# Kernel optimization log

Hardware: AMD Instinct MI355X
Metric: run time of the kernel (lower is better)

Reference implementation:

```python
import jax, jax.numpy as jnp
import numpy as np

N_SRC = 50000   # source nodes in the block
N_DST = 50000   # destination nodes
E = 800000      # edges (avg in-degree 16, every dst has >=1 edge)
D = 256         # hidden_dim
V = 50000       # vocab_size
C = 104         # n_classes (POJ-104)


def setup_inputs() -> dict:
    key = jax.random.key(0)
    k1, k2, k3, k4, k5, k6 = jax.random.split(key, 6)
    token_id = jax.random.randint(k1, (N_SRC,), 0, V, dtype=jnp.int32)
    src_idx = jax.random.randint(k2, (E,), 0, N_SRC, dtype=jnp.int32)
    # every dst node gets at least one in-edge (DGL raises on 0-in-degree),
    # remaining edges land on random dst nodes; sorted so edges are grouped by dst
    extra = jax.random.randint(k3, (E - N_DST,), 0, N_DST, dtype=jnp.int32)
    dst_idx = jnp.sort(jnp.concatenate([jnp.arange(N_DST, dtype=jnp.int32), extra]))
    emb = jax.random.normal(k4, (V, D), dtype=jnp.float32)  # nn.Embedding default N(0,1)
    W = jax.random.normal(k5, (D, D), dtype=jnp.float32) / jnp.sqrt(D)
    b = jnp.zeros((D,), dtype=jnp.float32)
    Wc = jax.random.normal(k6, (C, D), dtype=jnp.float32) / jnp.sqrt(D)
    bc = jnp.zeros((C,), dtype=jnp.float32)
    return {"emb": emb, "W": W, "b": b, "Wc": Wc, "bc": bc,
            "token_id": token_id, "src_idx": src_idx, "dst_idx": dst_idx}


def reference(emb, W, b, Wc, bc, token_id, src_idx, dst_idx):
    # embedding gather for source nodes (first_layer branch)
    feat_src = emb[token_id]                  # [N_SRC, D]
    # message: copy_u -> mailbox messages per edge
    msgs = feat_src[src_idx]                  # [E, D]
    # per-dst segment stats (dst_idx is sorted / grouped by dst)
    deg = jax.ops.segment_sum(jnp.ones((E,), dtype=jnp.int32), dst_idx,
                              num_segments=N_DST)            # [N_DST]
    sum_all = jax.ops.segment_sum(msgs, dst_idx, num_segments=N_DST)  # [N_DST, D]
    # DGL mailbox reducer: last message in the segment is the 'current input',
    # the rest are children summed through CodeRNNCell: x = cur + relu(W @ sum_children + b)
    last_idx = jnp.cumsum(deg) - 1            # index of last edge per dst segment
    last_msg = msgs[last_idx]                 # [N_DST, D]
    child_sum = sum_all - last_msg            # sum of msgs excluding the last one
    rnn_out = last_msg + jax.nn.relu(child_sum @ W.T + b)
    # length == 1 segments bypass the RNN cell entirely: ft = the single message
    ft = jnp.where((deg == 1)[:, None], last_msg, rnn_out)   # [N_DST, D]
    # final classifier
    return ft @ Wc.T + bc                     # [N_DST, C]
```

## Files before the change

kernel.cpp:

```cpp
#include <hip/hip_runtime.h>
#include <hip/hip_bf16.h>

#define DD 256
#define CC 104

typedef __bf16 bf16x8 __attribute__((ext_vector_type(8)));
typedef float  f32x4  __attribute__((ext_vector_type(4)));

__device__ inline unsigned short f2bu(float f) {
    __hip_bfloat16 h = __float2bfloat16(f);
    return *reinterpret_cast<unsigned short*>(&h);
}
__device__ inline float b2f(__hip_bfloat16 h) { return __bfloat162float(h); }

__global__ void prep_kernel(const int* __restrict__ token_id,
                            const int* __restrict__ src_idx,
                            const int* __restrict__ dst_idx,
                            int* __restrict__ seg_start,
                            int* __restrict__ seg_end,
                            int* __restrict__ edge_tok,
                            int E)
{
    int e = blockIdx.x * blockDim.x + threadIdx.x;
    if (e >= E) return;
    int d = dst_idx[e];
    edge_tok[e] = token_id[src_idx[e]];
    if (e == 0 || dst_idx[e - 1] != d) seg_start[d] = e;
    if (e == E - 1 || dst_idx[e + 1] != d) seg_end[d] = e + 1;
}

__global__ void convert_kernel(const float* __restrict__ emb,
                               const float* __restrict__ W,
                               const float* __restrict__ Wc,
                               __hip_bfloat16* __restrict__ embb,
                               __hip_bfloat16* __restrict__ Wb,
                               __hip_bfloat16* __restrict__ Wcb,
                               int nE4)
{
    const int nW4  = DD * DD / 4;
    const int nWc4 = 128 * DD / 4;
    int i = blockIdx.x * blockDim.x + threadIdx.x;
    float4 v;
    __hip_bfloat16* dst;
    if (i < nE4) {
        v = ((const float4*)emb)[i];
        dst = embb + (size_t)i * 4;
    } else if (i < nE4 + nW4) {
        int j = i - nE4;
        v = ((const float4*)W)[j];
        dst = Wb + (size_t)j * 4;
    } else if (i < nE4 + nW4 + nWc4) {
        int j = i - nE4 - nW4;
        v = (j < CC * DD / 4) ? ((const float4*)Wc)[j]
                              : make_float4(0.f, 0.f, 0.f, 0.f);
        dst = Wcb + (size_t)j * 4;
    } else return;
    ushort4 o;
    o.x = f2bu(v.x); o.y = f2bu(v.y); o.z = f2bu(v.z); o.w = f2bu(v.w);
    *(ushort4*)dst = o;
}

__global__ void seg_sum_kernel(const __hip_bfloat16* __restrict__ embb,
                               const int* __restrict__ edge_tok,
                               const int* __restrict__ seg_start,
                               const int* __restrict__ seg_end,
                               __hip_bfloat16* __restrict__ childb,
                               int n_dst)
{
    int w = (blockIdx.x * blockDim.x + threadIdx.x) >> 6;
    int lane = threadIdx.x & 63;
    if (w >= n_dst) return;
    int h   = lane >> 5;
    int l32 = lane & 31;
    int s = seg_start[w];
    int e = seg_end[w] - 1;
    float acc[8] = {0.f,0.f,0.f,0.f,0.f,0.f,0.f,0.f};

    auto accum = [&](int tok) {
        uint4 u = *(const uint4*)(embb + (size_t)tok * DD + l32 * 8);
        const unsigned* ud = (const unsigned*)&u;
#pragma unroll
        for (int d = 0; d < 4; ++d) {
            acc[2*d]   += __uint_as_float(ud[d] << 16);
            acc[2*d+1] += __uint_as_float(ud[d] & 0xffff0000u);
        }
    };

    int i = s + h;
    for (; i + 2 < e; i += 4) {
        int t0 = edge_tok[i];
        int t1 = edge_tok[i + 2];
        uint4 u0 = *(const uint4*)(embb + (size_t)t0 * DD + l32 * 8);
        uint4 u1 = *(const uint4*)(embb + (size_t)t1 * DD + l32 * 8);
        const unsigned* a0 = (const unsigned*)&u0;
        const unsigned* a1 = (const unsigned*)&u1;
#pragma unroll
        for (int d = 0; d < 4; ++d) {
            acc[2*d]   += __uint_as_float(a0[d] << 16) + __uint_as_float(a1[d] << 16);
            acc[2*d+1] += __uint_as_float(a0[d] & 0xffff0000u) + __uint_as_float(a1[d] & 0xffff0000u);
        }
    }
    if (i < e) accum(edge_tok[i]);

#pragma unroll
    for (int j = 0; j < 8; ++j) acc[j] += __shfl_xor(acc[j], 32, 64);

    if (h == 0) {
        uint4 o;
        unsigned* od = (unsigned*)&o;
#pragma unroll
        for (int d = 0; d < 4; ++d)
            od[d] = (unsigned)f2bu(acc[2*d]) | ((unsigned)f2bu(acc[2*d+1]) << 16);
        *(uint4*)(childb + (size_t)w * DD + l32 * 8) = o;
    }
}

#define FT_STRIDE 264
__global__ __launch_bounds__(256, 3) void rnn_cls_mfma(
    const __hip_bfloat16* __restrict__ childb,
    const __hip_bfloat16* __restrict__ Wb,
    const float* __restrict__ bvec,
    const __hip_bfloat16* __restrict__ Wcb,
    const float* __restrict__ bc,
    const __hip_bfloat16* __restrict__ embb,
    const int* __restrict__ seg_start,
    const int* __restrict__ seg_end,
    const int* __restrict__ edge_tok,
    float* __restrict__ out,
    int M)
{
    extern __shared__ char smem[];
    __hip_bfloat16* lds = (__hip_bfloat16*)smem;
    const int t    = threadIdx.x;
    const int lane = t & 63;
    const int wid  = t >> 6;
    const int quad = lane >> 4;
    const int l16  = lane & 15;
    const int m0   = blockIdx.x * 64;
    const int mw   = m0 + wid * 16;

    bool multi[4];
#pragma unroll
    for (int r = 0; r < 4; ++r) {
        int m = min(mw + quad * 4 + r, M - 1);
        multi[r] = (seg_end[m] - seg_start[m]) > 1;
    }
    int mrow = min(mw + l16, M - 1);
    int ltok = edge_tok[seg_end[mrow] - 1];

    const __hip_bfloat16* arow = childb + (size_t)mrow * DD + quad * 8;
    bf16x8 afrag[8];
#pragma unroll
    for (int k = 0; k < 8; ++k)
        afrag[k] = *(const bf16x8*)(arow + k * 32);

    float bias[16];
#pragma unroll
    for (int nt = 0; nt < 16; ++nt) bias[nt] = bvec[nt * 16 + l16];

    f32x4 acc[16];
#pragma unroll
    for (int nt = 0; nt < 16; ++nt) acc[nt] = (f32x4){0.f,0.f,0.f,0.f};

    for (int p = 0; p < 4; ++p) {
        __syncthreads();
#pragma unroll
        for (int it = 0; it < 8; ++it) {
            int idx = it * 256 + t;
            int g = idx >> 6, s = idx & 63;
            int nt = g & 15, kl = g >> 4;
            int row = nt * 16 + (s & 15);
            int col = (p * 2 + kl) * 32 + (s >> 4) * 8;
            *(bf16x8*)(lds + g * 512 + s * 8) =
                *(const bf16x8*)(Wb + (size_t)row * DD + col);
        }
        __syncthreads();
#pragma unroll
        for (int kl = 0; kl < 2; ++kl) {
            bf16x8 a = afrag[p * 2 + kl];
#pragma unroll
            for (int nt = 0; nt < 16; ++nt) {
                bf16x8 b = *(const bf16x8*)(lds + (kl * 16 + nt) * 512 + lane * 8);
                acc[nt] = __builtin_amdgcn_mfma_f32_16x16x32_bf16(a, b, acc[nt], 0, 0, 0);
            }
        }
    }

    __syncthreads();
#pragma unroll
    for (int nt = 0; nt < 16; ++nt) {
#pragma unroll
        for (int r = 0; r < 4; ++r) {
            float v = multi[r] ? fmaxf(acc[nt][r] + bias[nt], 0.f) : 0.f;
            lds[(wid * 16 + quad * 4 + r) * FT_STRIDE + nt * 16 + l16] =
                __float2bfloat16(v);
        }
    }
    __syncthreads();

    const __hip_bfloat16* lrow = embb + (size_t)ltok * DD + quad * 8;
    bf16x8 ftfrag[8];
#pragma unroll
    for (int k = 0; k < 8; ++k) {
        bf16x8 rp = *(const bf16x8*)(lds + (wid * 16 + l16) * FT_STRIDE + k * 32 + quad * 8);
        bf16x8 lm = *(const bf16x8*)(lrow + k * 32);
        bf16x8 o;
#pragma unroll
        for (int j = 0; j < 8; ++j)
            o[j] = (__bf16)(__bf16)((float)rp[j] + (float)lm[j]);
        ftfrag[k] = o;
    }

    f32x4 acc2[8];
#pragma unroll
    for (int nt = 0; nt < 8; ++nt) acc2[nt] = (f32x4){0.f,0.f,0.f,0.f};

    for (int p = 0; p < 2; ++p) {
        __syncthreads();
#pragma unroll
        for (int it = 0; it < 8; ++it) {
            int idx = it * 256 + t;
            int g = idx >> 6, s = idx & 63;
            int nt = g & 7, kt = g >> 3;
            int row = nt * 16 + (s & 15);
            int col = (p * 4 + kt) * 32 + (s >> 4) * 8;
            *(bf16x8*)(lds + g * 512 + s * 8) =
                *(const bf16x8*)(Wcb + (size_t)row * DD + col);
        }
        __syncthreads();
#pragma unroll
        for (int kt = 0; kt < 4; ++kt) {
            bf16x8 a = ftfrag[p * 4 + kt];
#pragma unroll
            for (int nt = 0; nt < 8; ++nt) {
                bf16x8 b = *(const bf16x8*)(lds + (kt * 8 + nt) * 512 + lane * 8);
                acc2[nt] = __builtin_amdgcn_mfma_f32_16x16x32_bf16(a, b, acc2[nt], 0, 0, 0);
            }
        }
    }

    float bcv[8];
#pragma unroll
    for (int nt = 0; nt < 8; ++nt) {
        int c = nt * 16 + l16;
        bcv[nt] = (c < CC) ? bc[c] : 0.f;
    }
#pragma unroll
    for (int r = 0; r < 4; ++r) {
        int m = mw + quad * 4 + r;
        if (m < M) {
#pragma unroll
            for (int nt = 0; nt < 8; ++nt) {
                int c = nt * 16 + l16;
                if (c < CC)
                    out[(size_t)m * CC + c] = acc2[nt][r] + bcv[nt];
            }
        }
    }
}

extern "C" void kernel_launch(void* const* d_in, const int* in_sizes, int n_in,
                              void* d_out, int out_size, void* d_ws, size_t ws_size,
                              hipStream_t stream)
{
    const float* emb      = (const float*)d_in[0];
    const float* W        = (const float*)d_in[1];
    const float* bvec     = (const float*)d_in[2];
    const float* Wc       = (const float*)d_in[3];
    const float* bc       = (const float*)d_in[4];
    const int*   token_id = (const int*)d_in[5];
    const int*   src_idx  = (const int*)d_in[6];
    const int*   dst_idx  = (const int*)d_in[7];
    float*       out      = (float*)d_out;

    const int E     = in_sizes[6];
    const int Vemb  = in_sizes[0] / DD;
    const int n_dst = out_size / CC;
    (void)n_in; (void)ws_size;

    char* ws = (char*)d_ws;
    size_t off = 0;
    auto alloc = [&](size_t bytes) {
        void* p = ws + off;
        off = (off + bytes + 255) & ~(size_t)255;
        return p;
    };
    int* seg_start = (int*)alloc((size_t)n_dst * sizeof(int));
    int* seg_end   = (int*)alloc((size_t)n_dst * sizeof(int));
    int* edge_tok  = (int*)alloc((size_t)E * sizeof(int));
    __hip_bfloat16* childb = (__hip_bfloat16*)alloc((size_t)n_dst * DD * 2);
    __hip_bfloat16* embb   = (__hip_bfloat16*)alloc((size_t)Vemb * DD * 2);
    __hip_bfloat16* Wb     = (__hip_bfloat16*)alloc((size_t)DD * DD * 2);
    __hip_bfloat16* Wcb    = (__hip_bfloat16*)alloc((size_t)128 * DD * 2);

    const int nE4 = Vemb * (DD / 4);
    const int cvt_total = nE4 + DD * DD / 4 + 128 * DD / 4;
    const int fused_blocks = (n_dst + 63) / 64;
    const int lds_bytes = 64 * FT_STRIDE * 2;

    prep_kernel<<<(E + 255) / 256, 256, 0, stream>>>(
        token_id, src_idx, dst_idx, seg_start, seg_end, edge_tok, E);
    convert_kernel<<<(cvt_total + 255) / 256, 256, 0, stream>>>(
        emb, W, Wc, embb, Wb, Wcb, nE4);
    seg_sum_kernel<<<(n_dst + 3) / 4, 256, 0, stream>>>(
        embb, edge_tok, seg_start, seg_end, childb, n_dst);
    rnn_cls_mfma<<<fused_blocks, 256, lds_bytes, stream>>>(
        childb, Wb, bvec, Wcb, bc, embb, seg_start, seg_end, edge_tok,
        out, n_dst);
}
```

Baseline: 207.0 us.

## Fuse segment-sum into MFMA kernel and pre-swizzle weights into fragment layout

```diff
diff --git a/kernel.cpp b/kernel.cpp
--- a/kernel.cpp
+++ b/kernel.cpp
@@ -3,257 +3,237 @@
 
 #define DD 256
 #define CC 104
+#define FT_STRIDE 264
 
 typedef __bf16 bf16x8 __attribute__((ext_vector_type(8)));
 typedef float  f32x4  __attribute__((ext_vector_type(4)));
 
+__device__ inline float bu2f(unsigned short u) {
+    return __uint_as_float(((unsigned)u) << 16);
+}
 __device__ inline unsigned short f2bu(float f) {
     __hip_bfloat16 h = __float2bfloat16(f);
     return *reinterpret_cast<unsigned short*>(&h);
 }
-__device__ inline float b2f(__hip_bfloat16 h) { return __bfloat162float(h); }
-
-__global__ void prep_kernel(const int* __restrict__ token_id,
-                            const int* __restrict__ src_idx,
-                            const int* __restrict__ dst_idx,
-                            int* __restrict__ seg_start,
-                            int* __restrict__ seg_end,
-                            int* __restrict__ edge_tok,
-                            int E)
+
+__global__ void prep_all(
+    const int* __restrict__ token_id,
+    const int* __restrict__ src_idx,
+    const int* __restrict__ dst_idx,
+    int* __restrict__ seg_start,
+    int* __restrict__ seg_end,
+    int* __restrict__ edge_tok,
+    int E, int PB,
+    const float* __restrict__ W,
+    const float* __restrict__ Wc,
+    __hip_bfloat16* __restrict__ Wfrag,
+    __hip_bfloat16* __restrict__ Wcfrag,
+    const float* __restrict__ emb,
+    __hip_bfloat16* __restrict__ embb,
+    int nE4)
 {
-    int e = blockIdx.x * blockDim.x + threadIdx.x;
-    if (e >= E) return;
-    int d = dst_idx[e];
-    edge_tok[e] = token_id[src_idx[e]];
-    if (e == 0 || dst_idx[e - 1] != d) seg_start[d] = e;
-    if (e == E - 1 || dst_idx[e + 1] != d) seg_end[d] = e + 1;
-}
-
-__global__ void convert_kernel(const float* __restrict__ emb,
-                               const float* __restrict__ W,
-                               const float* __restrict__ Wc,
-                               __hip_bfloat16* __restrict__ embb,
-                               __hip_bfloat16* __restrict__ Wb,
-                               __hip_bfloat16* __restrict__ Wcb,
-                               int nE4)
-{
-    const int nW4  = DD * DD / 4;
-    const int nWc4 = 128 * DD / 4;
-    int i = blockIdx.x * blockDim.x + threadIdx.x;
-    float4 v;
-    __hip_bfloat16* dst;
-    if (i < nE4) {
-        v = ((const float4*)emb)[i];
-        dst = embb + (size_t)i * 4;
-    } else if (i < nE4 + nW4) {
-        int j = i - nE4;
-        v = ((const float4*)W)[j];
-        dst = Wb + (size_t)j * 4;
-    } else if (i < nE4 + nW4 + nWc4) {
-        int j = i - nE4 - nW4;
-        v = (j < CC * DD / 4) ? ((const float4*)Wc)[j]
-                              : make_float4(0.f, 0.f, 0.f, 0.f);
-        dst = Wcb + (size_t)j * 4;
-    } else return;
+    const int b = blockIdx.x;
+    const int t = threadIdx.x;
+    if (b < PB) {
+        int e = b * 256 + t;
+        if (e >= E) return;
+        int d = dst_idx[e];
+        edge_tok[e] = token_id[src_idx[e]];
+        if (e == 0 || dst_idx[e - 1] != d) seg_start[d] = e;
+        if (e == E - 1 || dst_idx[e + 1] != d) seg_end[d] = e + 1;
+        return;
+    }
+    if (b < PB + 32) {
+        int idx  = (b - PB) * 256 + t;
+        int lane = idx & 63, g = idx >> 6;
+        int nt = g & 15, k0 = g >> 4;
+        int r = nt * 16 + (lane & 15);
+        int c = k0 * 32 + (lane >> 4) * 8;
+        const float* src = W + (size_t)r * DD + c;
+        float4 v0 = *(const float4*)(src);
+        float4 v1 = *(const float4*)(src + 4);
+        uint4 pk;
+        pk.x = (unsigned)f2bu(v0.x) | ((unsigned)f2bu(v0.y) << 16);
+        pk.y = (unsigned)f2bu(v0.z) | ((unsigned)f2bu(v0.w) << 16);
+        pk.z = (unsigned)f2bu(v1.x) | ((unsigned)f2bu(v1.y) << 16);
+        pk.w = (unsigned)f2bu(v1.z) | ((unsigned)f2bu(v1.w) << 16);
+        *(uint4*)(Wfrag + (size_t)idx * 8) = pk;
+        return;
+    }
+    if (b < PB + 48) {
+        int idx  = (b - PB - 32) * 256 + t;
+        int lane = idx & 63, g = idx >> 6;
+        int nt = g & 7, k0 = g >> 3;
+        int r = nt * 16 + (lane & 15);
+        int c = k0 * 32 + (lane >> 4) * 8;
+        float4 v0 = make_float4(0.f,0.f,0.f,0.f);
+        float4 v1 = make_float4(0.f,0.f,0.f,0.f);
+        if (r < CC) {
+            const float* src = Wc + (size_t)r * DD + c;
+            v0 = *(const float4*)(src);
+            v1 = *(const float4*)(src + 4);
+        }
+        uint4 pk;
+        pk.x = (unsigned)f2bu(v0.x) | ((unsigned)f2bu(v0.y) << 16);
+        pk.y = (unsigned)f2bu(v0.z) | ((unsigned)f2bu(v0.w) << 16);
+        pk.z = (unsigned)f2bu(v1.x) | ((unsigned)f2bu(v1.y) << 16);
+        pk.w = (unsigned)f2bu(v1.z) | ((unsigned)f2bu(v1.w) << 16);
+        *(uint4*)(Wcfrag + (size_t)idx * 8) = pk;
+        return;
+    }
+    int i = (b - PB - 48) * 256 + t;
+    if (i >= nE4) return;
+    float4 v = ((const float4*)emb)[i];
     ushort4 o;
     o.x = f2bu(v.x); o.y = f2bu(v.y); o.z = f2bu(v.z); o.w = f2bu(v.w);
-    *(ushort4*)dst = o;
-}
-
-__global__ void seg_sum_kernel(const __hip_bfloat16* __restrict__ embb,
-                               const int* __restrict__ edge_tok,
-                               const int* __restrict__ seg_start,
-                               const int* __restrict__ seg_end,
-                               __hip_bfloat16* __restrict__ childb,
-                               int n_dst)
-{
-    int w = (blockIdx.x * blockDim.x + threadIdx.x) >> 6;
-    int lane = threadIdx.x & 63;
-    if (w >= n_dst) return;
-    int h   = lane >> 5;
-    int l32 = lane & 31;
-    int s = seg_start[w];
-    int e = seg_end[w] - 1;
-    float acc[8] = {0.f,0.f,0.f,0.f,0.f,0.f,0.f,0.f};
-
-    auto accum = [&](int tok) {
-        uint4 u = *(const uint4*)(embb + (size_t)tok * DD + l32 * 8);
-        const unsigned* ud = (const unsigned*)&u;
-#pragma unroll
-        for (int d = 0; d < 4; ++d) {
-            acc[2*d]   += __uint_as_float(ud[d] << 16);
-            acc[2*d+1] += __uint_as_float(ud[d] & 0xffff0000u);
-        }
-    };
-
-    int i = s + h;
-    for (; i + 2 < e; i += 4) {
-        int t0 = edge_tok[i];
-        int t1 = edge_tok[i + 2];
-        uint4 u0 = *(const uint4*)(embb + (size_t)t0 * DD + l32 * 8);
-        uint4 u1 = *(const uint4*)(embb + (size_t)t1 * DD + l32 * 8);
-        const unsigned* a0 = (const unsigned*)&u0;
-        const unsigned* a1 = (const unsigned*)&u1;
-#pragma unroll
-        for (int d = 0; d < 4; ++d) {
-            acc[2*d]   += __uint_as_float(a0[d] << 16) + __uint_as_float(a1[d] << 16);
-            acc[2*d+1] += __uint_as_float(a0[d] & 0xffff0000u) + __uint_as_float(a1[d] & 0xffff0000u);
-        }
-    }
-    if (i < e) accum(edge_tok[i]);
-
-#pragma unroll
-    for (int j = 0; j < 8; ++j) acc[j] += __shfl_xor(acc[j], 32, 64);
-
-    if (h == 0) {
-        uint4 o;
-        unsigned* od = (unsigned*)&o;
-#pragma unroll
-        for (int d = 0; d < 4; ++d)
-            od[d] = (unsigned)f2bu(acc[2*d]) | ((unsigned)f2bu(acc[2*d+1]) << 16);
-        *(uint4*)(childb + (size_t)w * DD + l32 * 8) = o;
-    }
-}
-
-#define FT_STRIDE 264
-__global__ __launch_bounds__(256, 3) void rnn_cls_mfma(
-    const __hip_bfloat16* __restrict__ childb,
-    const __hip_bfloat16* __restrict__ Wb,
-    const float* __restrict__ bvec,
-    const __hip_bfloat16* __restrict__ Wcb,
-    const float* __restrict__ bc,
+    *(ushort4*)(embb + (size_t)i * 4) = o;
+}
+
+__global__ __launch_bounds__(256, 3) void mega(
     const __hip_bfloat16* __restrict__ embb,
+    const int* __restrict__ edge_tok,
     const int* __restrict__ seg_start,
     const int* __restrict__ seg_end,
-    const int* __restrict__ edge_tok,
+    const __hip_bfloat16* __restrict__ Wfrag,
+    const float* __restrict__ bvec,
+    const __hip_bfloat16* __restrict__ Wcfrag,
+    const float* __restrict__ bc,
     float* __restrict__ out,
     int M)
 {
     extern __shared__ char smem[];
-    __hip_bfloat16* lds = (__hip_bfloat16*)smem;
+    __hip_bfloat16* child = (__hip_bfloat16*)smem;
     const int t    = threadIdx.x;
     const int lane = t & 63;
-    const int wid  = t >> 6;
+    const int w    = t >> 6;
     const int quad = lane >> 4;
     const int l16  = lane & 15;
-    const int m0   = blockIdx.x * 64;
-    const int mw   = m0 + wid * 16;
-
-    bool multi[4];
-#pragma unroll
-    for (int r = 0; r < 4; ++r) {
-        int m = min(mw + quad * 4 + r, M - 1);
-        multi[r] = (seg_end[m] - seg_start[m]) > 1;
-    }
-    int mrow = min(mw + l16, M - 1);
-    int ltok = edge_tok[seg_end[mrow] - 1];
-
-    const __hip_bfloat16* arow = childb + (size_t)mrow * DD + quad * 8;
-    bf16x8 afrag[8];
-#pragma unroll
-    for (int k = 0; k < 8; ++k)
-        afrag[k] = *(const bf16x8*)(arow + k * 32);
-
-    float bias[16];
-#pragma unroll
-    for (int nt = 0; nt < 16; ++nt) bias[nt] = bvec[nt * 16 + l16];
-
-    f32x4 acc[16];
-#pragma unroll
-    for (int nt = 0; nt < 16; ++nt) acc[nt] = (f32x4){0.f,0.f,0.f,0.f};
-
-    for (int p = 0; p < 4; ++p) {
-        __syncthreads();
-#pragma unroll
-        for (int it = 0; it < 8; ++it) {
-            int idx = it * 256 + t;
-            int g = idx >> 6, s = idx & 63;
-            int nt = g & 15, kl = g >> 4;
-            int row = nt * 16 + (s & 15);
-            int col = (p * 2 + kl) * 32 + (s >> 4) * 8;
-            *(bf16x8*)(lds + g * 512 + s * 8) =
-                *(const bf16x8*)(Wb + (size_t)row * DD + col);
-        }
-        __syncthreads();
-#pragma unroll
-        for (int kl = 0; kl < 2; ++kl) {
-            bf16x8 a = afrag[p * 2 + kl];
-#pragma unroll
-            for (int nt = 0; nt < 16; ++nt) {
-                bf16x8 b = *(const bf16x8*)(lds + (kl * 16 + nt) * 512 + lane * 8);
-                acc[nt] = __builtin_amdgcn_mfma_f32_16x16x32_bf16(a, b, acc[nt], 0, 0, 0);
+    const int h    = lane >> 5;
+    const int l32  = lane & 31;
+    const int rb   = w * 16;
+    const int mb   = blockIdx.x * 64 + rb;
+
+    int mm0 = min(mb + l16, M - 1);
+    int sA  = seg_start[mm0];
+    int eA  = seg_end[mm0];
+    int ltA = edge_tok[eA - 1];
+    bool muA = (eA - sA) > 1;
+
+    for (int j = 0; j < 16; ++j) {
+        int s = __shfl(sA, j, 64);
+        int e = __shfl(eA, j, 64) - 1;
+        float acc[8] = {0.f,0.f,0.f,0.f,0.f,0.f,0.f,0.f};
+        int i = s + h;
+        for (; i + 6 < e; i += 8) {
+            int t0 = edge_tok[i];
+            int t1 = edge_tok[i + 2];
+            int t2 = edge_tok[i + 4];
+            int t3 = edge_tok[i + 6];
+            uint4 u0 = *(const uint4*)(embb + (size_t)t0 * DD + l32 * 8);
+            uint4 u1 = *(const uint4*)(embb + (size_t)t1 * DD + l32 * 8);
+            uint4 u2 = *(const uint4*)(embb + (size_t)t2 * DD + l32 * 8);
+            uint4 u3 = *(const uint4*)(embb + (size_t)t3 * DD + l32 * 8);
+            const unsigned* a0 = (const unsigned*)&u0;
+            const unsigned* a1 = (const unsigned*)&u1;
+            const unsigned* a2 = (const unsigned*)&u2;
+            const unsigned* a3 = (const unsigned*)&u3;
+#pragma unroll
+            for (int d = 0; d < 4; ++d) {
+                acc[2*d]   += (__uint_as_float(a0[d] << 16) + __uint_as_float(a1[d] << 16))
+                            + (__uint_as_float(a2[d] << 16) + __uint_as_float(a3[d] << 16));
+                acc[2*d+1] += (__uint_as_float(a0[d] & 0xffff0000u) + __uint_as_float(a1[d] & 0xffff0000u))
+                            + (__uint_as_float(a2[d] & 0xffff0000u) + __uint_as_float(a3[d] & 0xffff0000u));
             }
         }
-    }
-
-    __syncthreads();
+        for (; i < e; i += 2) {
+            int t0 = edge_tok[i];
+            uint4 u = *(const uint4*)(embb + (size_t)t0 * DD + l32 * 8);
+            const unsigned* ud = (const unsigned*)&u;
+#pragma unroll
+            for (int d = 0; d < 4; ++d) {
+                acc[2*d]   += __uint_as_float(ud[d] << 16);
+                acc[2*d+1] += __uint_as_float(ud[d] & 0xffff0000u);
+            }
+        }
+#pragma unroll
+        for (int jj = 0; jj < 8; ++jj) acc[jj] += __shfl_xor(acc[jj], 32, 64);
+        if (h == 0) {
+            uint4 o;
+            unsigned* od = (unsigned*)&o;
+#pragma unroll
+            for (int d = 0; d < 4; ++d)
+                od[d] = (unsigned)f2bu(acc[2*d]) | ((unsigned)f2bu(acc[2*d+1]) << 16);
+            *(uint4*)(child + (rb + j) * FT_STRIDE + l32 * 8) = o;
+        }
+    }
+
+    const __hip_bfloat16* crow = child + (rb + l16) * FT_STRIDE + quad * 8;
+    bf16x8 cfrag[8];
+#pragma unroll
+    for (int k0 = 0; k0 < 8; ++k0)
+        cfrag[k0] = *(const bf16x8*)(crow + k0 * 32);
+
+    f32x4 acc1[16];
+#pragma unroll
+    for (int nt = 0; nt < 16; ++nt) acc1[nt] = (f32x4){0.f,0.f,0.f,0.f};
+#pragma unroll
+    for (int k0 = 0; k0 < 8; ++k0) {
+#pragma unroll
+        for (int nt = 0; nt < 16; ++nt) {
+            bf16x8 wf = *(const bf16x8*)(Wfrag + ((k0 * 16 + nt) * 512) + lane * 8);
+            acc1[nt] = __builtin_amdgcn_mfma_f32_16x16x32_bf16(wf, cfrag[k0], acc1[nt], 0, 0, 0);
+        }
+    }
+
 #pragma unroll
     for (int nt = 0; nt < 16; ++nt) {
-#pragma unroll
-        for (int r = 0; r < 4; ++r) {
-            float v = multi[r] ? fmaxf(acc[nt][r] + bias[nt], 0.f) : 0.f;
-            lds[(wid * 16 + quad * 4 + r) * FT_STRIDE + nt * 16 + l16] =
-                __float2bfloat16(v);
-        }
-    }
-    __syncthreads();
-
-    const __hip_bfloat16* lrow = embb + (size_t)ltok * DD + quad * 8;
-    bf16x8 ftfrag[8];
-#pragma unroll
-    for (int k = 0; k < 8; ++k) {
-        bf16x8 rp = *(const bf16x8*)(lds + (wid * 16 + l16) * FT_STRIDE + k * 32 + quad * 8);
-        bf16x8 lm = *(const bf16x8*)(lrow + k * 32);
+        float4 bia = *(const float4*)(bvec + nt * 16 + quad * 4);
+        ushort4 o;
+        o.x = f2bu(muA ? fmaxf(acc1[nt][0] + bia.x, 0.f) : 0.f);
+        o.y = f2bu(muA ? fmaxf(acc1[nt][1] + bia.y, 0.f) : 0.f);
+        o.z = f2bu(muA ? fmaxf(acc1[nt][2] + bia.z, 0.f) : 0.f);
+        o.w = f2bu(muA ? fmaxf(acc1[nt][3] + bia.w, 0.f) : 0.f);
+        *(ushort4*)(child + (rb + l16) * FT_STRIDE + nt * 16 + quad * 4) = o;
+    }
+
+    const __hip_bfloat16* lrow = embb + (size_t)ltA * DD + quad * 8;
+    bf16x8 ff[8];
+#pragma unroll
+    for (int k0 = 0; k0 < 8; ++k0) {
+        bf16x8 rp = *(const bf16x8*)(crow + k0 * 32);
+        bf16x8 lm = *(const bf16x8*)(lrow + k0 * 32);
         bf16x8 o;
 #pragma unroll
         for (int j = 0; j < 8; ++j)
-            o[j] = (__bf16)(__bf16)((float)rp[j] + (float)lm[j]);
-        ftfrag[k] = o;
+            o[j] = (__bf16)((float)rp[j] + (float)lm[j]);
+        ff[k0] = o;
     }
 
     f32x4 acc2[8];
 #pragma unroll
     for (int nt = 0; nt < 8; ++nt) acc2[nt] = (f32x4){0.f,0.f,0.f,0.f};
-
-    for (int p = 0; p < 2; ++p) {
-        __syncthreads();
-#pragma unroll
-        for (int it = 0; it < 8; ++it) {
-            int idx = it * 256 + t;
-            int g = idx >> 6, s = idx & 63;
-            int nt = g & 7, kt = g >> 3;
-            int row = nt * 16 + (s & 15);
-            int col = (p * 4 + kt) * 32 + (s >> 4) * 8;
-            *(bf16x8*)(lds + g * 512 + s * 8) =
-                *(const bf16x8*)(Wcb + (size_t)row * DD + col);
-        }
-        __syncthreads();
-#pragma unroll
-        for (int kt = 0; kt < 4; ++kt) {
-            bf16x8 a = ftfrag[p * 4 + kt];
-#pragma unroll
-            for (int nt = 0; nt < 8; ++nt) {
-                bf16x8 b = *(const bf16x8*)(lds + (kt * 8 + nt) * 512 + lane * 8);
-                acc2[nt] = __builtin_amdgcn_mfma_f32_16x16x32_bf16(a, b, acc2[nt], 0, 0, 0);
-            }
-        }
-    }
-
-    float bcv[8];
-#pragma unroll
-    for (int nt = 0; nt < 8; ++nt) {
-        int c = nt * 16 + l16;
-        bcv[nt] = (c < CC) ? bc[c] : 0.f;
-    }
-#pragma unroll
-    for (int r = 0; r < 4; ++r) {
-        int m = mw + quad * 4 + r;
-        if (m < M) {
-#pragma unroll
-            for (int nt = 0; nt < 8; ++nt) {
-                int c = nt * 16 + l16;
-                if (c < CC)
-                    out[(size_t)m * CC + c] = acc2[nt][r] + bcv[nt];
+#pragma unroll
+    for (int k0 = 0; k0 < 8; ++k0) {
+#pragma unroll
+        for (int nt = 0; nt < 8; ++nt) {
+            bf16x8 wcf = *(const bf16x8*)(Wcfrag + ((k0 * 8 + nt) * 512) + lane * 8);
+            acc2[nt] = __builtin_amdgcn_mfma_f32_16x16x32_bf16(wcf, ff[k0], acc2[nt], 0, 0, 0);
+        }
+    }
+
+    int m = mb + l16;
+    if (m < M) {
+#pragma unroll
+        for (int nt = 0; nt < 8; ++nt) {
+            int c0 = nt * 16 + quad * 4;
+            if (c0 <= 100) {
+                float4 bia = *(const float4*)(bc + c0);
+                float4 o;
+                o.x = acc2[nt][0] + bia.x;
+                o.y = acc2[nt][1] + bia.y;
+                o.z = acc2[nt][2] + bia.z;
+                o.w = acc2[nt][3] + bia.w;
+                *(float4*)(out + (size_t)m * CC + c0) = o;
             }
         }
     }
@@ -288,23 +268,20 @@
     int* seg_start = (int*)alloc((size_t)n_dst * sizeof(int));
     int* seg_end   = (int*)alloc((size_t)n_dst * sizeof(int));
     int* edge_tok  = (int*)alloc((size_t)E * sizeof(int));
-    __hip_bfloat16* childb = (__hip_bfloat16*)alloc((size_t)n_dst * DD * 2);
     __hip_bfloat16* embb   = (__hip_bfloat16*)alloc((size_t)Vemb * DD * 2);
-    __hip_bfloat16* Wb     = (__hip_bfloat16*)alloc((size_t)DD * DD * 2);
-    __hip_bfloat16* Wcb    = (__hip_bfloat16*)alloc((size_t)128 * DD * 2);
+    __hip_bfloat16* Wfrag  = (__hip_bfloat16*)alloc((size_t)128 * 512 * 2);
+    __hip_bfloat16* Wcfrag = (__hip_bfloat16*)alloc((size_t)64 * 512 * 2);
 
     const int nE4 = Vemb * (DD / 4);
-    const int cvt_total = nE4 + DD * DD / 4 + 128 * DD / 4;
-    const int fused_blocks = (n_dst + 63) / 64;
+    const int PB  = (E + 255) / 256;
+    const int cvtB = (nE4 + 255) / 256;
+    const int mega_blocks = (n_dst + 63) / 64;
     const int lds_bytes = 64 * FT_STRIDE * 2;
 
-    prep_kernel<<<(E + 255) / 256, 256, 0, stream>>>(
-        token_id, src_idx, dst_idx, seg_start, seg_end, edge_tok, E);
-    convert_kernel<<<(cvt_total + 255) / 256, 256, 0, stream>>>(
-        emb, W, Wc, embb, Wb, Wcb, nE4);
-    seg_sum_kernel<<<(n_dst + 3) / 4, 256, 0, stream>>>(
-        embb, edge_tok, seg_start, seg_end, childb, n_dst);
-    rnn_cls_mfma<<<fused_blocks, 256, lds_bytes, stream>>>(
-        childb, Wb, bvec, Wcb, bc, embb, seg_start, seg_end, edge_tok,
+    prep_all<<<PB + 48 + cvtB, 256, 0, stream>>>(
+        token_id, src_idx, dst_idx, seg_start, seg_end, edge_tok, E, PB,
+        W, Wc, Wfrag, Wcfrag, emb, embb, nE4);
+    mega<<<mega_blocks, 256, lds_bytes, stream>>>(
+        embb, edge_tok, seg_start, seg_end, Wfrag, bvec, Wcfrag, bc,
         out, n_dst);
 }
```

New measurement: 237.7 us. 1.15x slower.
